# Performance work log

Hardware: AMD Instinct MI355X
Metric: run time of the kernel (lower is better)

## Reference

```python
import jax, jax.numpy as jnp
import numpy as np

P = 7    # pool size (hard-coded in module)
DS = 16  # downsample rate


def _hat_int(t):
    # antiderivative of the bilinear hat kernel max(0, 1-|t|)
    t = jnp.clip(t, -1.0, 1.0)
    return jnp.where(t < 0, 0.5 * (t + 1.0) ** 2, 1.0 - 0.5 * (1.0 - t) ** 2)


def _axis_weights(lo, hi, size):
    # Exact per-pixel integration weights for PrRoIPool along one axis.
    # lo, hi: [R] scaled roi coords. Returns W [R,P,size], bin width [R].
    bw = (hi - lo) / P
    starts = lo[:, None] + bw[:, None] * jnp.arange(P, dtype=lo.dtype)  # [R,P]
    ends = starts + bw[:, None]
    idx = jnp.arange(size, dtype=lo.dtype)
    W = _hat_int(ends[:, :, None] - idx) - _hat_int(starts[:, :, None] - idx)
    return W, bw


def prroi_pool(feat, rois):
    # Precise RoI pooling: exact integral of the bilinearly-interpolated feature
    # over each bin (separable -> two small matmuls). feat [C,H,W], rois [R,4].
    C, H, Wd = feat.shape
    s = 1.0 / DS
    Wx, bw = _axis_weights(rois[:, 0] * s, rois[:, 2] * s, Wd)
    Wy, bh = _axis_weights(rois[:, 1] * s, rois[:, 3] * s, H)
    pooled = jnp.einsum('chw,rph,rqw->rcpq', feat, Wy, Wx)  # [R,C,P,P]
    area = jnp.maximum(bw * bh, 1e-8)
    return pooled / area[:, None, None, None]


def intersection_map(box1, box2):
    # Fractional coverage of each PxP bin of box2's grid by box1 -> [N,1,P,P]
    bw = (box2[:, 2] - box2[:, 0]) / P
    bh = (box2[:, 3] - box2[:, 1]) / P
    gx0 = box2[:, 0, None] + bw[:, None] * jnp.arange(P)
    gy0 = box2[:, 1, None] + bh[:, None] * jnp.arange(P)
    ox = jnp.clip(jnp.minimum(gx0 + bw[:, None], box1[:, 2, None]) - jnp.maximum(gx0, box1[:, 0, None]), 0.0)
    oy = jnp.clip(jnp.minimum(gy0 + bh[:, None], box1[:, 3, None]) - jnp.maximum(gy0, box1[:, 1, None]), 0.0)
    frac = oy[:, :, None] * ox[:, None, :] / jnp.maximum(bw * bh, 1e-8)[:, None, None]
    return frac[:, None]


def conv1x1(x, W, b):
    # 1x1 conv as a channel matmul; x [...,C,H,W], W [D,C], b [D]
    return jnp.einsum('...chw,dc->...dhw', x, W) + b[:, None, None]


def setup_inputs() -> dict:
    key = jax.random.key(0)
    ks = jax.random.split(key, 12)
    B, C, Hf, Wf, n = 8, 256, 32, 32, 16
    D1 = D2 = 256
    inp = jax.random.normal(ks[0], (B, C, Hf, Wf), dtype=jnp.float32)
    N = B * n
    xy1 = jax.random.uniform(ks[1], (N, 2), dtype=jnp.float32) * 380.0
    wh = 40.0 + jax.random.uniform(ks[2], (N, 2), dtype=jnp.float32) * 90.0
    objects = jnp.concatenate([xy1, xy1 + wh], axis=-1)  # valid boxes inside 512x512
    objects_length = jnp.full((B,), n, dtype=jnp.int32)

    def kaiming(k, shape, fan_in):
        return jax.random.normal(k, shape, dtype=jnp.float32) * np.float32(np.sqrt(2.0 / fan_in))

    rin = C // 2 * 3 + 2 * D1
    return {
        'input': inp, 'objects': objects, 'objects_length': objects_length,
        'Wc': kaiming(ks[3], (C, C), C), 'bc': jnp.zeros((C,), jnp.float32),
        'Wr': kaiming(ks[4], (C // 2 * 3, C), C), 'br': jnp.zeros((C // 2 * 3,), jnp.float32),
        'Wof': kaiming(ks[5], (D1, 2 * C), 2 * C), 'bof': jnp.zeros((D1,), jnp.float32),
        'Wrf': kaiming(ks[6], (D2, rin), rin), 'brf': jnp.zeros((D2,), jnp.float32),
        'Wofc': kaiming(ks[7], (D1, D1 * P * P), D1 * P * P), 'bofc': jnp.zeros((D1,), jnp.float32),
        'Wrfc': kaiming(ks[8], (D2, D2 * P * P), D2 * P * P), 'brfc': jnp.zeros((D2,), jnp.float32),
    }


def reference(input, objects, objects_length, Wc, bc, Wr, br, Wof, bof, Wrf, brf, Wofc, bofc, Wrfc, brfc):
    B, C, H, Wd = input.shape
    n = objects.shape[0] // B  # uniform object count per image
    boxes = objects.reshape(B, n, 4)
    ctx_all = conv1x1(input, Wc, bc)           # [B,C,H,W]
    rel_all = conv1x1(input, Wr, br)           # [B,3C/2,H,W]
    img_box = jnp.array([0.0, 0.0, Wd * DS, H * DS], dtype=input.dtype)
    sub_id = jnp.repeat(jnp.arange(n), n)
    obj_id = jnp.tile(jnp.arange(n), n)

    def per_image(feat, ctx, rel, box):
        # context pooled over the full-image box is identical for all objects
        ctx_pool = prroi_pool(ctx, img_box[None])[0]                    # [C,P,P]
        x_c, y_c = jnp.split(ctx_pool, 2, axis=0)
        box_imap = jax.lax.stop_gradient(
            intersection_map(box, jnp.broadcast_to(img_box, (n, 4))))  # [n,1,P,P]
        obj_pool = prroi_pool(feat, box)                                # [n,C,P,P]
        obj_in = jnp.concatenate([
            obj_pool,
            jnp.broadcast_to(x_c, (n,) + x_c.shape),
            y_c[None] * box_imap], axis=1)                              # [n,2C,P,P]
        obj_feat = conv1x1(obj_in, Wof, bof)                            # [n,D1,P,P]

        sub_box, ob_box = box[sub_id], box[obj_id]                      # [n*n,4]
        union = jax.lax.stop_gradient(jnp.concatenate(
            [jnp.minimum(sub_box[:, :2], ob_box[:, :2]),
             jnp.maximum(sub_box[:, 2:], ob_box[:, 2:])], axis=-1))
        sub_imap = jax.lax.stop_gradient(intersection_map(sub_box, union))
        obj_imap = jax.lax.stop_gradient(intersection_map(ob_box, union))
        rel_pool = prroi_pool(rel, union)                               # [n*n,3C/2,P,P]
        xr, yr, zr = jnp.split(rel_pool, 3, axis=1)
        rel_in = jnp.concatenate([
            obj_feat[sub_id], obj_feat[obj_id],
            xr, yr * sub_imap, zr * obj_imap], axis=1)                  # [n*n,2D1+3C/2,P,P]
        rel_feat = conv1x1(rel_in, Wrf, brf)                            # [n*n,D2,P,P]

        o = jax.nn.relu(obj_feat).reshape(n, -1) @ Wofc.T + bofc
        o = o / jnp.linalg.norm(o, axis=-1, keepdims=True)
        r = jax.nn.relu(rel_feat).reshape(n * n, -1) @ Wrfc.T + brfc
        r = r / jnp.linalg.norm(r, axis=-1, keepdims=True)
        return o, r.reshape(n, n, -1)

    obj_out, rel_out = jax.vmap(per_image)(input, ctx_all, rel_all, boxes)
    return obj_out, rel_out
```

## Files before the change

kernel.cpp:

```cpp
#include <hip/hip_runtime.h>
#include <hip/hip_bf16.h>


#define Bimg 8
#define Cch 256
#define HW 1024
#define CREL 384
#define CCAT 640
#define KFC 12544
#define STS 236

typedef __hip_bfloat16 bf16;
typedef __attribute__((ext_vector_type(8))) short short8;
typedef __attribute__((ext_vector_type(4))) short short4_t;
typedef __attribute__((ext_vector_type(4))) float f32x4;

__device__ __forceinline__ float hat_int(float t) {
    t = fminf(1.f, fmaxf(-1.f, t));
    return (t < 0.f) ? 0.5f * (t + 1.f) * (t + 1.f) : 1.f - 0.5f * (1.f - t) * (1.f - t);
}
__device__ __forceinline__ float b2f(short s) {
    return __uint_as_float(((unsigned)(unsigned short)s) << 16);
}
__device__ __forceinline__ unsigned pack2bf(float a, float b) {
    bf16 ha = __float2bfloat16(a), hb = __float2bfloat16(b);
    return ((unsigned)(unsigned short)(*(short*)&hb) << 16) | (unsigned short)(*(short*)&ha);
}

__global__ void prep_k(const float* __restrict__ Wc, const float* __restrict__ bc,
                       const float* __restrict__ Wr, const float* __restrict__ br,
                       bf16* __restrict__ Wcat, float* __restrict__ bcat,
                       const float* __restrict__ Wof, bf16* __restrict__ wof16,
                       const float* __restrict__ Wrf, bf16* __restrict__ wasao16,
                       bf16* __restrict__ wrfxyz16) {
    int bid = blockIdx.x, tid = threadIdx.x;
    if (bid < 640) {
        int t = bid * 256 + tid;
        int d = t >> 8, c = t & 255;
        Wcat[t] = __float2bfloat16((d < 256) ? Wc[d * 256 + c] : Wr[(d - 256) * 256 + c]);
        if (t < CCAT) bcat[t] = (t < 256) ? bc[t] : br[t - 256];
    } else if (bid < 1152) {
        int t = (bid - 640) * 256 + tid;
        wof16[t] = __float2bfloat16(Wof[t]);
    } else if (bid < 1664) {
        int t = (bid - 1152) * 256 + tid;
        int m = t >> 8, k = t & 255;
        wasao16[t] = __float2bfloat16((m < 256) ? Wrf[m * 896 + k] : Wrf[(m - 256) * 896 + 256 + k]);
    } else {
        int t = (bid - 1664) * 256 + tid;
        int d = t / 384, k = t - d * 384;
        wrfxyz16[t] = __float2bfloat16(Wrf[d * 896 + 512 + k]);
    }
}
__global__ __launch_bounds__(256) void wfc_pack_k(const float* __restrict__ W, bf16* __restrict__ dst) {
    __shared__ float ld[64 * 50];
    int dout = blockIdx.y, d0 = blockIdx.x * 64;
    int tid = threadIdx.x;
    for (int e = tid; e < 64 * 49; e += 256) {
        int di = e / 49, pq = e - di * 49;
        ld[di * 50 + pq] = W[(size_t)dout * KFC + (d0 + di) * 49 + pq];
    }
    __syncthreads();
    for (int e = tid; e < 64 * 49; e += 256) {
        int pq = e >> 6, di = e & 63;
        if (pq < 49)
            dst[(size_t)dout * KFC + pq * 256 + d0 + di] = __float2bfloat16(ld[di * 50 + pq]);
    }
}

__global__ void axisw_k(const float* __restrict__ objects,
                        float* __restrict__ orec, float* __restrict__ urec,
                        float* __restrict__ crec, float* __restrict__ bimap) {
    int bid = blockIdx.x;
    float b0, b1, b2, b3;
    float* rec;
    const float *sbp = nullptr, *obp = nullptr;
    if (bid < 128) {
        b0 = objects[bid * 4]; b1 = objects[bid * 4 + 1];
        b2 = objects[bid * 4 + 2]; b3 = objects[bid * 4 + 3];
        rec = orec + (size_t)bid * 128;
    } else if (bid < 2176) {
        int u = bid - 128;
        int img = u >> 8, pair = u & 255, i = pair >> 4, j = pair & 15;
        sbp = objects + (img * 16 + i) * 4;
        obp = objects + (img * 16 + j) * 4;
        b0 = fminf(sbp[0], obp[0]); b1 = fminf(sbp[1], obp[1]);
        b2 = fmaxf(sbp[2], obp[2]); b3 = fmaxf(sbp[3], obp[3]);
        rec = urec + (size_t)(u) * 224;
    } else {
        b0 = 0.f; b1 = 0.f; b2 = 512.f; b3 = 512.f;
        rec = crec;
    }
    const float sc = 0.0625f;
    float lox = b0 * sc, bwx = (b2 * sc - lox) * (1.f / 7.f);
    float loy = b1 * sc, bwy = (b3 * sc - loy) * (1.f / 7.f);
    float ia = 1.f / fmaxf(bwx * bwy, 1e-8f);
    int tid = threadIdx.x;
    if (tid < 56) {
        int p = tid >> 3, k = tid & 7;
        {
            float st = loy + bwy * p, en = st + bwy;
            int h0 = min(max((int)floorf(st) - 1, 0), 24);
            rec[tid] = hat_int(en - (float)(h0 + k)) - hat_int(st - (float)(h0 + k));
            if (k == 0) ((int*)rec)[119 + p] = h0;
        }
        {
            float st = lox + bwx * p, en = st + bwx;
            int w0 = min(max((int)floorf(st) - 1, 0), 24);
            rec[56 + tid] = ia * (hat_int(en - (float)(w0 + k)) - hat_int(st - (float)(w0 + k)));
            if (k == 0) ((int*)rec)[112 + p] = w0;
        }
    }
    if (tid < 49) {
        int p = tid / 7, q = tid - p * 7;
        if (bid < 128) {
            float bw = 512.f / 7.f, bh = 512.f / 7.f;
            float gx0 = bw * q, gy0 = bh * p;
            float ox = fmaxf(fminf(gx0 + bw, b2) - fmaxf(gx0, b0), 0.f);
            float oy = fmaxf(fminf(gy0 + bh, b3) - fmaxf(gy0, b1), 0.f);
            bimap[bid * 49 + tid] = oy * ox / fmaxf(bw * bh, 1e-8f);
        } else if (bid < 2176) {
            float bw = (b2 - b0) * (1.f / 7.f), bh = (b3 - b1) * (1.f / 7.f);
            float gx0 = b0 + bw * q, gy0 = b1 + bh * p;
            float inv = 1.f / fmaxf(bw * bh, 1e-8f);
            float oxs = fmaxf(fminf(gx0 + bw, sbp[2]) - fmaxf(gx0, sbp[0]), 0.f);
            float oys = fmaxf(fminf(gy0 + bh, sbp[3]) - fmaxf(gy0, sbp[1]), 0.f);
            rec[126 + tid] = oys * oxs * inv;
            float oxo = fmaxf(fminf(gx0 + bw, obp[2]) - fmaxf(gx0, obp[0]), 0.f);
            float oyo = fmaxf(fminf(gy0 + bh, obp[3]) - fmaxf(gy0, obp[1]), 0.f);
            rec[175 + tid] = oyo * oxo * inv;
        }
    }
}

__global__ __launch_bounds__(256) void int_t_k(const float* __restrict__ input, bf16* __restrict__ intp) {
    __shared__ float st[64][65];
    int hw0 = blockIdx.x * 64, c0 = blockIdx.y * 64, b = blockIdx.z;
    int tid = threadIdx.x;
#pragma unroll
    for (int i = 0; i < 16; i++) {
        int e = tid + i * 256;
        int c = e >> 6, hw = e & 63;
        st[c][hw] = input[(size_t)b * 262144 + (size_t)(c0 + c) * 1024 + hw0 + hw];
    }
    __syncthreads();
#pragma unroll
    for (int i = 0; i < 16; i++) {
        int e = tid + i * 256;
        int hw = e >> 6, c = e & 63;
        intp[((size_t)b * 1024 + hw0 + hw) * 256 + c0 + c] = __float2bfloat16(st[c][hw]);
    }
}

__global__ __launch_bounds__(256) void mfma_gemm_k(
    const bf16* __restrict__ A, int lda,
    const bf16* __restrict__ BT, int ldbt,
    int Ktiles, int splitk, int mode,
    float* __restrict__ Cf, int Mtot, int Ntot,
    const float* __restrict__ bias,
    bf16* __restrict__ Ct, int ldct, bf16* __restrict__ Ct2) {
    __shared__ float tr[32 * 132];
    const int tid = threadIdx.x;
    const int m0 = blockIdx.y * 128, n0 = blockIdx.x * 128;
    int kz = blockIdx.z;
    const int tp = (Ktiles + splitk - 1) / splitk;
    const int kt0 = kz * tp;
    const int kt1 = min(Ktiles, kt0 + tp);
    const int lane = tid & 63, wid = tid >> 6;
    const int wm = (wid >> 1) * 64, wn = (wid & 1) * 64;
    const int lrow = lane & 15, lk = (lane >> 4) * 8;
    f32x4 acc[4][4];
#pragma unroll
    for (int i = 0; i < 4; i++)
#pragma unroll
        for (int j = 0; j < 4; j++) acc[i][j] = (f32x4){0.f, 0.f, 0.f, 0.f};
    const bf16* pA = A + (size_t)(m0 + wm + lrow) * lda + lk;
    const bf16* pB = BT + (size_t)(n0 + wn + lrow) * ldbt + lk;
    short8 a_c[4], b_c[4];
    if (kt0 < kt1) {
#pragma unroll
        for (int f = 0; f < 4; f++) {
            a_c[f] = *(const short8*)(pA + (size_t)f * 16 * lda + (size_t)kt0 * 32);
            b_c[f] = *(const short8*)(pB + (size_t)f * 16 * ldbt + (size_t)kt0 * 32);
        }
    }
    for (int kt = kt0; kt < kt1; kt++) {
        short8 a_n[4], b_n[4];
        if (kt + 1 < kt1) {
#pragma unroll
            for (int f = 0; f < 4; f++) {
                a_n[f] = *(const short8*)(pA + (size_t)f * 16 * lda + (size_t)(kt + 1) * 32);
                b_n[f] = *(const short8*)(pB + (size_t)f * 16 * ldbt + (size_t)(kt + 1) * 32);
            }
        }
#pragma unroll
        for (int i = 0; i < 4; i++)
#pragma unroll
            for (int j = 0; j < 4; j++)
                acc[i][j] = __builtin_amdgcn_mfma_f32_16x16x32_bf16(a_c[i], b_c[j], acc[i][j], 0, 0, 0);
#pragma unroll
        for (int f = 0; f < 4; f++) { a_c[f] = a_n[f]; b_c[f] = b_n[f]; }
    }
    const int rbase = (lane >> 4) * 4, cf = lane & 15;
    if (mode == 5) {
#pragma unroll
        for (int i = 0; i < 4; i++)
#pragma unroll
            for (int reg = 0; reg < 4; reg++) {
                int m = m0 + wm + i * 16 + rbase + reg;
                float bv = bias[m];
#pragma unroll
                for (int j = 0; j < 4; j++) {
                    int n = n0 + wn + j * 16 + cf;
                    Ct[(size_t)m * ldct + n] = __float2bfloat16(acc[i][j][reg] + bv);
                }
            }
        return;
    }
#pragma unroll 1
    for (int ci = 0; ci < 4; ci++) {
        __syncthreads();
        if ((wid & 1) == (ci >> 1)) {
            int jj0 = (ci & 1) * 2;
#pragma unroll
            for (int jj = jj0; jj < jj0 + 2; jj++)
#pragma unroll
                for (int i = 0; i < 4; i++)
#pragma unroll
                    for (int reg = 0; reg < 4; reg++) {
                        int nl = (wn + jj * 16 + cf) - 32 * ci;
                        int ml = wm + i * 16 + rbase + reg;
                        tr[nl * 132 + ml] = acc[i][jj][reg];
                    }
        }
        __syncthreads();
        if (mode == 2) {
            float* P = Cf + (size_t)kz * Mtot * Ntot;
            for (int e = tid; e < 1024; e += 256) {
                int nl = e >> 5, mq = (e & 31) * 4;
                int n = n0 + 32 * ci + nl;
                *(f32x4*)&P[(size_t)n * Mtot + m0 + mq] = *(f32x4*)&tr[nl * 132 + mq];
            }
        } else {
            for (int e = tid; e < 2048; e += 256) {
                int nl = e >> 6, mq = (e & 63) * 2;
                int n = n0 + 32 * ci + nl;
                int m = m0 + mq;
                float v0 = tr[nl * 132 + mq] + (bias ? bias[m] : 0.f);
                float v1 = tr[nl * 132 + mq + 1] + (bias ? bias[m + 1] : 0.f);
                *(unsigned*)&Ct[(size_t)n * ldct + m] = pack2bf(v0, v1);
                if (mode == 6) {
                    int r = n / 49, pq = n - r * 49;
                    *(unsigned*)&Ct2[(size_t)r * KFC + pq * 256 + m] =
                        pack2bf(fmaxf(v0, 0.f), fmaxf(v1, 0.f));
                }
            }
        }
    }
}

__global__ __launch_bounds__(256) void mfma_gemm256_k(
    const bf16* __restrict__ A, int lda,
    const bf16* __restrict__ BT, int ldbt, long zB,
    int Ktiles, int splitk, int mode,
    float* __restrict__ Cf, int Ntot,
    const float* __restrict__ bias,
    const bf16* __restrict__ ASAOT, int bimg0,
    bf16* __restrict__ Ct, long zC) {
    __shared__ float tr[16 * 260];
    const int tid = threadIdx.x;
    const int n0 = blockIdx.x * 64;
    int z = blockIdx.z;
    int kz = 0, bimg = bimg0;
    if (mode == 1) { BT += (size_t)z * zB; Ct += (size_t)z * zC; bimg = bimg0 + z; }
    else kz = z;
    const int tp = (Ktiles + splitk - 1) / splitk;
    const int kt0 = kz * tp;
    const int kt1 = min(Ktiles, kt0 + tp);
    const int lane = tid & 63, wid = tid >> 6;
    const int wm = wid * 64;
    const int lrow = lane & 15, lk = (lane >> 4) * 8;
    f32x4 acc[4][4];
#pragma unroll
    for (int i = 0; i < 4; i++)
#pragma unroll
        for (int j = 0; j < 4; j++) acc[i][j] = (f32x4){0.f, 0.f, 0.f, 0.f};
    const bf16* pA = A + (size_t)(wm + lrow) * lda + lk;
    const bf16* pB = (mode == 1)
        ? BT + (size_t)(lk >> 3) * 100352 + (size_t)(n0 + lrow) * 8
        : BT + (size_t)(n0 + lrow) * ldbt + lk;
    short8 a_c[4], b_c[4];
    if (kt0 < kt1) {
#pragma unroll
        for (int f = 0; f < 4; f++) {
            a_c[f] = *(const short8*)(pA + (size_t)f * 16 * lda + (size_t)kt0 * 32);
            b_c[f] = (mode == 1)
                ? *(const short8*)(pB + (size_t)kt0 * 4 * 100352 + f * 128)
                : *(const short8*)(pB + (size_t)f * 16 * ldbt + (size_t)kt0 * 32);
        }
    }
    for (int kt = kt0; kt < kt1; kt++) {
        short8 a_n[4], b_n[4];
        if (kt + 1 < kt1) {
#pragma unroll
            for (int f = 0; f < 4; f++) {
                a_n[f] = *(const short8*)(pA + (size_t)f * 16 * lda + (size_t)(kt + 1) * 32);
                b_n[f] = (mode == 1)
                    ? *(const short8*)(pB + (size_t)(kt + 1) * 4 * 100352 + f * 128)
                    : *(const short8*)(pB + (size_t)f * 16 * ldbt + (size_t)(kt + 1) * 32);
            }
        }
#pragma unroll
        for (int i = 0; i < 4; i++)
#pragma unroll
            for (int j = 0; j < 4; j++)
                acc[i][j] = __builtin_amdgcn_mfma_f32_16x16x32_bf16(a_c[i], b_c[j], acc[i][j], 0, 0, 0);
#pragma unroll
        for (int f = 0; f < 4; f++) { a_c[f] = a_n[f]; b_c[f] = b_n[f]; }
    }
    const int rbase = (lane >> 4) * 4, cf = lane & 15;
#pragma unroll 1
    for (int ci = 0; ci < 4; ci++) {
        __syncthreads();
#pragma unroll
        for (int i = 0; i < 4; i++)
#pragma unroll
            for (int reg = 0; reg < 4; reg++)
                tr[cf * 260 + wm + i * 16 + rbase + reg] = acc[i][ci][reg];
        __syncthreads();
        if (mode == 2) {
            float* P = Cf + (size_t)kz * 256 * Ntot;
            for (int e = tid; e < 1024; e += 256) {
                int nl = e >> 6, mq = (e & 63) * 4;
                int n = n0 + 16 * ci + nl;
                *(f32x4*)&P[(size_t)n * 256 + mq] = *(f32x4*)&tr[nl * 260 + mq];
            }
        } else {
            for (int e = tid; e < 512; e += 256) {
                int nl = e >> 5, mq = (e & 31) * 8;
                int n = n0 + 16 * ci + nl;
                int r = n / 49, pq = n - r * 49;
                int ii = r >> 4, jj2 = r & 15;
                const bf16* as = &ASAOT[((size_t)bimg * 784 + ii * 49 + pq) * 512 + mq];
                const bf16* ao = &ASAOT[((size_t)bimg * 784 + jj2 * 49 + pq) * 512 + 256 + mq];
                short8 pk;
#pragma unroll
                for (int u = 0; u < 8; u++) {
                    float v = tr[nl * 260 + mq + u] + bias[mq + u]
                            + b2f(*(const short*)&as[u]) + b2f(*(const short*)&ao[u]);
                    bf16 h = __float2bfloat16(fmaxf(v, 0.f));
                    pk[u] = *(short*)&h;
                }
                *(short8*)&Ct[(size_t)r * KFC + pq * 256 + mq] = pk;
            }
        }
    }
}

__global__ __launch_bounds__(256) void objpool_k(
    const float* __restrict__ input, const float* __restrict__ orec,
    bf16* __restrict__ objint) {
    int cg = blockIdx.x;
    int b = blockIdx.y;
    __shared__ float sF[8192];
    __shared__ float sT[2][1888];
    __shared__ float wb[2][128];
    int tid = threadIdx.x;
    const float* feat = input + (size_t)b * (Cch * HW) + (size_t)cg * 8 * HW;
    for (int e4 = tid; e4 < 2048; e4 += 256)
        *(f32x4*)&sF[e4 * 4] = *(const f32x4*)&feat[e4 * 4];
    const float* rb = orec + (size_t)b * 16 * 128;
    if (tid < 126) wb[0][tid] = rb[tid];
    int t1v = tid + 256;
    int c0 = tid / 56, r0 = tid - c0 * 56, p0 = r0 >> 3, w40 = r0 & 7;
    int c1 = t1v / 56, r1 = t1v - c1 * 56, p1 = r1 >> 3, w41 = r1 & 7;
    bool has1 = (t1v < 448);
    int sf0 = c0 * 1024 + w40 * 4, st0 = c0 * STS + p0 * 32 + w40 * 4;
    int sf1 = c1 * 1024 + w41 * 4, st1 = c1 * STS + p1 * 32 + w41 * 4;
    int xpq0 = tid >> 3, xc = tid & 7;
    int xp0 = xpq0 / 7, xq0 = xpq0 - xp0 * 7;
    int xpq1 = xpq0 + 32;
    int xp1 = xpq1 / 7, xq1 = xpq1 - xp1 * 7;
    bool xv1 = (xpq1 < 49);
    __syncthreads();
    for (int r2 = 0; r2 < 16; r2++) {
        const float* wc_ = wb[r2 & 1];
        float* stbuf = sT[r2 & 1];
        float pre;
        bool pf = (r2 < 15) && (tid < 126);
        if (pf) pre = rb[(r2 + 1) * 128 + tid];
        {
            int h0 = ((const int*)wc_)[119 + p0];
            const f32x4* f = (const f32x4*)&sF[sf0 + h0 * 32];
            f32x4 wya = *(const f32x4*)&wc_[p0 * 8];
            f32x4 wyb = *(const f32x4*)&wc_[p0 * 8 + 4];
            f32x4 a = f[0] * wya[0] + f[8] * wya[1] + f[16] * wya[2] + f[24] * wya[3]
                    + f[32] * wyb[0] + f[40] * wyb[1] + f[48] * wyb[2] + f[56] * wyb[3];
            *(f32x4*)&stbuf[st0] = a;
        }
        if (has1) {
            int h0 = ((const int*)wc_)[119 + p1];
            const f32x4* f = (const f32x4*)&sF[sf1 + h0 * 32];
            f32x4 wya = *(const f32x4*)&wc_[p1 * 8];
            f32x4 wyb = *(const f32x4*)&wc_[p1 * 8 + 4];
            f32x4 a = f[0] * wya[0] + f[8] * wya[1] + f[16] * wya[2] + f[24] * wya[3]
                    + f[32] * wyb[0] + f[40] * wyb[1] + f[48] * wyb[2] + f[56] * wyb[3];
            *(f32x4*)&stbuf[st1] = a;
        }
        f32x4 xwa0 = *(const f32x4*)&wc_[56 + xq0 * 8];
        f32x4 xwb0 = *(const f32x4*)&wc_[56 + xq0 * 8 + 4];
        int w0i0 = ((const int*)wc_)[112 + xq0];
        f32x4 xwa1 = {0, 0, 0, 0}, xwb1 = {0, 0, 0, 0};
        int w0i1 = 0;
        if (xv1) {
            xwa1 = *(const f32x4*)&wc_[56 + xq1 * 8];
            xwb1 = *(const f32x4*)&wc_[56 + xq1 * 8 + 4];
            w0i1 = ((const int*)wc_)[112 + xq1];
        }
        if (pf) wb[1 - (r2 & 1)][tid] = pre;
        __syncthreads();
        {
            bf16* orow = objint + ((size_t)b * 784 + (size_t)r2 * 49) * 512 + cg * 8 + xc;
            {
                const float* t = &stbuf[xc * STS + xp0 * 32 + w0i0];
                float s = t[0] * xwa0[0] + t[1] * xwa0[1] + t[2] * xwa0[2] + t[3] * xwa0[3]
                        + t[4] * xwb0[0] + t[5] * xwb0[1] + t[6] * xwb0[2] + t[7] * xwb0[3];
                orow[(size_t)xpq0 * 512] = __float2bfloat16(s);
            }
            if (xv1) {
                const float* t = &stbuf[xc * STS + xp1 * 32 + w0i1];
                float s = t[0] * xwa1[0] + t[1] * xwa1[1] + t[2] * xwa1[2] + t[3] * xwa1[3]
                        + t[4] * xwb1[0] + t[5] * xwb1[1] + t[6] * xwb1[2] + t[7] * xwb1[3];
                orow[(size_t)xpq1 * 512] = __float2bfloat16(s);
            }
        }
    }
}

__global__ __launch_bounds__(256) void ctxobjin_k(
    const bf16* __restrict__ ctxrelb, const float* __restrict__ crec,
    const float* __restrict__ bimap, bf16* __restrict__ objint) {
    int cg = blockIdx.x;
    int b = blockIdx.y;
    __shared__ float sF[8192];
    __shared__ float sT[1888];
    __shared__ float wc_[128];
    __shared__ float sBI[784];
    int tid = threadIdx.x;
    for (int e4 = tid; e4 < 2048; e4 += 256) {
        short4_t v = *(const short4_t*)&ctxrelb[(size_t)(cg * 8 + (e4 >> 8)) * 8192 + b * 1024 + (e4 & 255) * 4];
        f32x4 fv = {b2f(v[0]), b2f(v[1]), b2f(v[2]), b2f(v[3])};
        *(f32x4*)&sF[e4 * 4] = fv;
    }
    if (tid < 126) wc_[tid] = crec[tid];
    for (int e = tid; e < 784; e += 256) sBI[e] = bimap[b * 784 + e];
    __syncthreads();
    for (int tt = tid; tt < 448; tt += 256) {
        int c = tt / 56, r = tt - c * 56, p = r >> 3, w4 = r & 7;
        int h0 = ((const int*)wc_)[119 + p];
        const f32x4* f = (const f32x4*)&sF[c * 1024 + w4 * 4 + h0 * 32];
        f32x4 wya = *(const f32x4*)&wc_[p * 8];
        f32x4 wyb = *(const f32x4*)&wc_[p * 8 + 4];
        f32x4 a = f[0] * wya[0] + f[8] * wya[1] + f[16] * wya[2] + f[24] * wya[3]
                + f[32] * wyb[0] + f[40] * wyb[1] + f[48] * wyb[2] + f[56] * wyb[3];
        *(f32x4*)&sT[c * STS + p * 32 + w4 * 4] = a;
    }
    __syncthreads();
    bool scale = (cg >= 16);
    for (int e = tid; e < 392; e += 256) {
        int pq = e >> 3, c = e & 7;
        int p = pq / 7, q = pq - p * 7;
        int w0i = ((const int*)wc_)[112 + q];
        const float* t = &sT[c * STS + p * 32 + w0i];
        const f32x4* wx4 = (const f32x4*)&wc_[56 + q * 8];
        f32x4 a = wx4[0], b2 = wx4[1];
        float s = t[0] * a[0] + t[1] * a[1] + t[2] * a[2] + t[3] * a[3]
                + t[4] * b2[0] + t[5] * b2[1] + t[6] * b2[2] + t[7] * b2[3];
        int j = cg * 8 + c;
        bf16* orow = objint + ((size_t)b * 784 + pq) * 512 + 256 + j;
#pragma unroll
        for (int r = 0; r < 16; r++) {
            float m = scale ? sBI[r * 49 + pq] : 1.f;
            orow[(size_t)r * 49 * 512] = __float2bfloat16(s * m);
        }
    }
}

__global__ __launch_bounds__(256) void relpool_k(
    const bf16* __restrict__ ctxrelb, const float* __restrict__ urec,
    bf16* __restrict__ mbt, int b0) {
    int cg = blockIdx.x;
    int rg = blockIdx.y;
    int zi = blockIdx.z;
    int b = b0 + zi;
    mbt += (size_t)zi * 4816896;
    __shared__ float sF[8192];
    __shared__ float sT[2][1888];
    __shared__ float wb[2][224];
    int tid = threadIdx.x;
    for (int e4 = tid; e4 < 2048; e4 += 256) {
        short4_t v = *(const short4_t*)&ctxrelb[(size_t)(256 + cg * 8 + (e4 >> 8)) * 8192 + b * 1024 + (e4 & 255) * 4];
        f32x4 fv = {b2f(v[0]), b2f(v[1]), b2f(v[2]), b2f(v[3])};
        *(f32x4*)&sF[e4 * 4] = fv;
    }
    const float* rb = urec + ((size_t)b * 256 + (size_t)rg * 16) * 224;
    if (tid < 224) wb[0][tid] = rb[tid];
    int t1v = tid + 256;
    int c0 = tid / 56, r0 = tid - c0 * 56, p0 = r0 >> 3, w40 = r0 & 7;
    int c1 = t1v / 56, r1 = t1v - c1 * 56, p1 = r1 >> 3, w41 = r1 & 7;
    bool has1 = (t1v < 448);
    int sf0 = c0 * 1024 + w40 * 4, st0 = c0 * STS + p0 * 32 + w40 * 4;
    int sf1 = c1 * 1024 + w41 * 4, st1 = c1 * STS + p1 * 32 + w41 * 4;
    int xpq0 = tid >> 3, xc = tid & 7;
    int xp0 = xpq0 / 7, xq0 = xpq0 - xp0 * 7;
    int xpq1 = xpq0 + 32;
    int xp1 = xpq1 / 7, xq1 = xpq1 - xp1 * 7;
    bool xv1 = (xpq1 < 49);
    int cglob = cg * 8 + xc;
    int mclass = (cglob >= 256) ? 2 : (cglob >= 128 ? 1 : 0);
    __syncthreads();
    for (int r2 = 0; r2 < 16; r2++) {
        const float* wc_ = wb[r2 & 1];
        float* stbuf = sT[r2 & 1];
        float pre;
        bool pf = (r2 < 15) && (tid < 224);
        if (pf) pre = rb[(r2 + 1) * 224 + tid];
        {
            int h0 = ((const int*)wc_)[119 + p0];
            const f32x4* f = (const f32x4*)&sF[sf0 + h0 * 32];
            f32x4 wya = *(const f32x4*)&wc_[p0 * 8];
            f32x4 wyb = *(const f32x4*)&wc_[p0 * 8 + 4];
            f32x4 a = f[0] * wya[0] + f[8] * wya[1] + f[16] * wya[2] + f[24] * wya[3]
                    + f[32] * wyb[0] + f[40] * wyb[1] + f[48] * wyb[2] + f[56] * wyb[3];
            *(f32x4*)&stbuf[st0] = a;
        }
        if (has1) {
            int h0 = ((const int*)wc_)[119 + p1];
            const f32x4* f = (const f32x4*)&sF[sf1 + h0 * 32];
            f32x4 wya = *(const f32x4*)&wc_[p1 * 8];
            f32x4 wyb = *(const f32x4*)&wc_[p1 * 8 + 4];
            f32x4 a = f[0] * wya[0] + f[8] * wya[1] + f[16] * wya[2] + f[24] * wya[3]
                    + f[32] * wyb[0] + f[40] * wyb[1] + f[48] * wyb[2] + f[56] * wyb[3];
            *(f32x4*)&stbuf[st1] = a;
        }
        f32x4 xwa0 = *(const f32x4*)&wc_[56 + xq0 * 8];
        f32x4 xwb0 = *(const f32x4*)&wc_[56 + xq0 * 8 + 4];
        int w0i0 = ((const int*)wc_)[112 + xq0];
        float mul0 = (mclass == 2) ? wc_[175 + xpq0] : (mclass == 1 ? wc_[126 + xpq0] : 1.f);
        f32x4 xwa1 = {0, 0, 0, 0}, xwb1 = {0, 0, 0, 0};
        int w0i1 = 0;
        float mul1 = 1.f;
        if (xv1) {
            xwa1 = *(const f32x4*)&wc_[56 + xq1 * 8];
            xwb1 = *(const f32x4*)&wc_[56 + xq1 * 8 + 4];
            w0i1 = ((const int*)wc_)[112 + xq1];
            mul1 = (mclass == 2) ? wc_[175 + xpq1] : (mclass == 1 ? wc_[126 + xpq1] : 1.f);
        }
        if (pf) wb[1 - (r2 & 1)][tid] = pre;
        __syncthreads();
        {
            int r = rg * 16 + r2;
            bf16* orow = mbt + (size_t)cg * 100352 + (size_t)r * 392;
            {
                const float* t = &stbuf[xc * STS + xp0 * 32 + w0i0];
                float s = t[0] * xwa0[0] + t[1] * xwa0[1] + t[2] * xwa0[2] + t[3] * xwa0[3]
                        + t[4] * xwb0[0] + t[5] * xwb0[1] + t[6] * xwb0[2] + t[7] * xwb0[3];
                orow[xpq0 * 8 + xc] = __float2bfloat16(s * mul0);
            }
            if (xv1) {
                const float* t = &stbuf[xc * STS + xp1 * 32 + w0i1];
                float s = t[0] * xwa1[0] + t[1] * xwa1[1] + t[2] * xwa1[2] + t[3] * xwa1[3]
                        + t[4] * xwb1[0] + t[5] * xwb1[1] + t[6] * xwb1[2] + t[7] * xwb1[3];
                orow[xpq1 * 8 + xc] = __float2bfloat16(s * mul1);
            }
        }
    }
}

__global__ void redns_k(const float* __restrict__ Pd, const float* __restrict__ bias,
                        float* __restrict__ out, int N, int splitk, long outBase) {
    int vec = blockIdx.x, m = threadIdx.x;
    float s = bias[m];
    for (int z = 0; z < splitk; z++) s += Pd[(size_t)z * 256 * N + (size_t)vec * 256 + m];
    float ss = s * s;
    for (int o = 32; o > 0; o >>= 1) ss += __shfl_down(ss, o, 64);
    __shared__ float red[4];
    if ((m & 63) == 0) red[m >> 6] = ss;
    __syncthreads();
    float tot = red[0] + red[1] + red[2] + red[3];
    out[outBase + (size_t)vec * 256 + m] = s / sqrtf(tot);
}

extern "C" void kernel_launch(void* const* d_in, const int* in_sizes, int n_in,
                              void* d_out, int out_size, void* d_ws, size_t ws_size,
                              hipStream_t stream) {
    const float* input = (const float*)d_in[0];
    const float* objects = (const float*)d_in[1];
    const float* Wc = (const float*)d_in[3];
    const float* bc = (const float*)d_in[4];
    const float* Wr = (const float*)d_in[5];
    const float* br = (const float*)d_in[6];
    const float* Wof = (const float*)d_in[7];
    const float* bof = (const float*)d_in[8];
    const float* Wrf = (const float*)d_in[9];
    const float* brf = (const float*)d_in[10];
    const float* Wofc = (const float*)d_in[11];
    const float* bofc = (const float*)d_in[12];
    const float* Wrfc = (const float*)d_in[13];
    const float* brfc = (const float*)d_in[14];
    float* out = (float*)d_out;

    float* w = (float*)d_ws;
    bf16* WCAT16   = (bf16*)(w + 0);
    float* BCAT    = w + 81920;
    bf16* CTXRELB  = (bf16*)(w + 82560);
    float* OREC    = w + 2704000;
    float* UREC    = w + 2720384;
    float* CREC    = w + 3179136;
    float* BIMAP   = w + 3179264;
    bf16* ASAOT16  = (bf16*)(w + 3185536);
    bf16* WRFXYZ16 = (bf16*)(w + 4791168);
    bf16* WRFC16   = (bf16*)(w + 4840320);
    float* OVL     = w + 6445952;
    bf16* INT16    = (bf16*)(OVL + 0);
    bf16* WOF16    = (bf16*)(OVL + 1048576);
    bf16* WASAO16  = (bf16*)(OVL + 1114112);
    bf16* WOFC16   = (bf16*)(OVL + 1179648);
    bf16* OBJINT   = (bf16*)(OVL + 2785280);
    bf16* OBJFT    = (bf16*)(OVL + 4390912);
    bf16* XOT      = (bf16*)(OVL + 5193728);
    float* OPART   = OVL + 5996544;
    bf16* MBT4     = (bf16*)(OVL + 0);
    float* RPART   = OVL + 0;
    bf16* XBT4     = (bf16*)(OVL + 9633792);

    prep_k<<<dim3(2048), 256, 0, stream>>>(Wc, bc, Wr, br, WCAT16, BCAT,
                                           Wof, WOF16, Wrf, WASAO16, WRFXYZ16);
    wfc_pack_k<<<dim3(4, 256), 256, 0, stream>>>(Wrfc, WRFC16);
    wfc_pack_k<<<dim3(4, 256), 256, 0, stream>>>(Wofc, WOFC16);
    axisw_k<<<dim3(2177), 64, 0, stream>>>(objects, OREC, UREC, CREC, BIMAP);
    int_t_k<<<dim3(16, 4, 8), 256, 0, stream>>>(input, INT16);
    mfma_gemm_k<<<dim3(64, 5, 1), 256, 0, stream>>>(WCAT16, 256, INT16, 256, 8, 1, 5,
                                                    nullptr, 640, 8192, BCAT,
                                                    CTXRELB, 8192, nullptr);
    objpool_k<<<dim3(32, 8), 256, 0, stream>>>(input, OREC, OBJINT);
    ctxobjin_k<<<dim3(32, 8), 256, 0, stream>>>(CTXRELB, CREC, BIMAP, OBJINT);
    mfma_gemm_k<<<dim3(49, 2, 1), 256, 0, stream>>>(WOF16, 512, OBJINT, 512, 16, 1, 6,
                                                    nullptr, 256, 6272, bof,
                                                    OBJFT, 256, XOT);
    mfma_gemm_k<<<dim3(49, 4, 1), 256, 0, stream>>>(WASAO16, 256, OBJFT, 256, 8, 1, 3,
                                                    nullptr, 512, 6272, nullptr,
                                                    ASAOT16, 512, nullptr);
    mfma_gemm_k<<<dim3(1, 2, 56), 256, 0, stream>>>(WOFC16, KFC, XOT, KFC, 392, 56, 2,
                                                    OPART, 256, 128, nullptr,
                                                    nullptr, 0, nullptr);
    redns_k<<<dim3(128), 256, 0, stream>>>(OPART, bofc, out, 128, 56, 0L);

    for (int g = 0; g < 2; g++) {
        int b0 = g * 4;
        relpool_k<<<dim3(48, 16, 4), 256, 0, stream>>>(CTXRELB, UREC, MBT4, b0);
        mfma_gemm256_k<<<dim3(196, 1, 4), 256, 0, stream>>>(WRFXYZ16, 384, MBT4, 384, 4816896L,
                                                            12, 1, 1,
                                                            nullptr, KFC, brf,
                                                            ASAOT16, b0, XBT4, 3211264L);
        mfma_gemm256_k<<<dim3(16, 1, 24), 256, 0, stream>>>(WRFC16, KFC, XBT4, KFC, 0L,
                                                            392, 24, 2,
                                                            RPART, 1024, nullptr,
                                                            nullptr, 0, nullptr, 0L);
        redns_k<<<dim3(1024), 256, 0, stream>>>(RPART, brfc, out, 1024, 24,
                                                32768L + (long)g * 262144L);
    }
}
```

Before: 652.1 us.

## Exploit union-box symmetry to pool each subject/object pair once in relpool

Result: faster. 618.4 us (median of 2 runs) (-5.2%).

```diff
diff --git a/kernel.cpp b/kernel.cpp
--- a/kernel.cpp
+++ b/kernel.cpp
@@ -25,6 +25,11 @@
 __device__ __forceinline__ unsigned pack2bf(float a, float b) {
     bf16 ha = __float2bfloat16(a), hb = __float2bfloat16(b);
     return ((unsigned)(unsigned short)(*(short*)&hb) << 16) | (unsigned short)(*(short*)&ha);
+}
+__device__ __forceinline__ void u2pair(int u, int& oi, int& oj) {
+    int ii = 0, base = 0;
+    while (u >= base + 16 - ii) { base += 16 - ii; ii++; }
+    oi = ii; oj = ii + (u - base);
 }
 
 __global__ void prep_k(const float* __restrict__ Wc, const float* __restrict__ bc,
@@ -503,8 +508,11 @@
         f32x4 fv = {b2f(v[0]), b2f(v[1]), b2f(v[2]), b2f(v[3])};
         *(f32x4*)&sF[e4 * 4] = fv;
     }
-    const float* rb = urec + ((size_t)b * 256 + (size_t)rg * 16) * 224;
-    if (tid < 224) wb[0][tid] = rb[tid];
+    const float* rb = urec + (size_t)b * 256 * 224;
+    {
+        int i0, j0; u2pair(rg * 8, i0, j0);
+        if (tid < 224) wb[0][tid] = rb[(size_t)(i0 * 16 + j0) * 224 + tid];
+    }
     int t1v = tid + 256;
     int c0 = tid / 56, r0 = tid - c0 * 56, p0 = r0 >> 3, w40 = r0 & 7;
     int c1 = t1v / 56, r1 = t1v - c1 * 56, p1 = r1 >> 3, w41 = r1 & 7;
@@ -519,12 +527,16 @@
     int cglob = cg * 8 + xc;
     int mclass = (cglob >= 256) ? 2 : (cglob >= 128 ? 1 : 0);
     __syncthreads();
-    for (int r2 = 0; r2 < 16; r2++) {
+    for (int r2 = 0; r2 < 8; r2++) {
         const float* wc_ = wb[r2 & 1];
         float* stbuf = sT[r2 & 1];
+        int pi, pj; u2pair(rg * 8 + r2, pi, pj);
         float pre;
-        bool pf = (r2 < 15) && (tid < 224);
-        if (pf) pre = rb[(r2 + 1) * 224 + tid];
+        bool pf = (r2 < 7) && (tid < 224);
+        if (pf) {
+            int ni, nj; u2pair(rg * 8 + r2 + 1, ni, nj);
+            pre = rb[(size_t)(ni * 16 + nj) * 224 + tid];
+        }
         {
             int h0 = ((const int*)wc_)[119 + p0];
             const f32x4* f = (const f32x4*)&sF[sf0 + h0 * 32];
@@ -546,32 +558,40 @@
         f32x4 xwa0 = *(const f32x4*)&wc_[56 + xq0 * 8];
         f32x4 xwb0 = *(const f32x4*)&wc_[56 + xq0 * 8 + 4];
         int w0i0 = ((const int*)wc_)[112 + xq0];
-        float mul0 = (mclass == 2) ? wc_[175 + xpq0] : (mclass == 1 ? wc_[126 + xpq0] : 1.f);
+        float si0 = wc_[126 + xpq0], oi0 = wc_[175 + xpq0];
+        float mA0 = (mclass == 1) ? si0 : (mclass == 2 ? oi0 : 1.f);
+        float mB0 = (mclass == 1) ? oi0 : (mclass == 2 ? si0 : 1.f);
         f32x4 xwa1 = {0, 0, 0, 0}, xwb1 = {0, 0, 0, 0};
         int w0i1 = 0;
-        float mul1 = 1.f;
+        float mA1 = 1.f, mB1 = 1.f;
         if (xv1) {
             xwa1 = *(const f32x4*)&wc_[56 + xq1 * 8];
             xwb1 = *(const f32x4*)&wc_[56 + xq1 * 8 + 4];
             w0i1 = ((const int*)wc_)[112 + xq1];
-            mul1 = (mclass == 2) ? wc_[175 + xpq1] : (mclass == 1 ? wc_[126 + xpq1] : 1.f);
+            float si1 = wc_[126 + xpq1], oi1 = wc_[175 + xpq1];
+            mA1 = (mclass == 1) ? si1 : (mclass == 2 ? oi1 : 1.f);
+            mB1 = (mclass == 1) ? oi1 : (mclass == 2 ? si1 : 1.f);
         }
         if (pf) wb[1 - (r2 & 1)][tid] = pre;
         __syncthreads();
         {
-            int r = rg * 16 + r2;
-            bf16* orow = mbt + (size_t)cg * 100352 + (size_t)r * 392;
+            int rA = pi * 16 + pj, rB = pj * 16 + pi;
+            bf16* baseA = mbt + (size_t)cg * 100352 + (size_t)rA * 392;
+            bf16* baseB = mbt + (size_t)cg * 100352 + (size_t)rB * 392;
+            bool dual = (pi != pj);
             {
                 const float* t = &stbuf[xc * STS + xp0 * 32 + w0i0];
                 float s = t[0] * xwa0[0] + t[1] * xwa0[1] + t[2] * xwa0[2] + t[3] * xwa0[3]
                         + t[4] * xwb0[0] + t[5] * xwb0[1] + t[6] * xwb0[2] + t[7] * xwb0[3];
-                orow[xpq0 * 8 + xc] = __float2bfloat16(s * mul0);
+                baseA[xpq0 * 8 + xc] = __float2bfloat16(s * mA0);
+                if (dual) baseB[xpq0 * 8 + xc] = __float2bfloat16(s * mB0);
             }
             if (xv1) {
                 const float* t = &stbuf[xc * STS + xp1 * 32 + w0i1];
                 float s = t[0] * xwa1[0] + t[1] * xwa1[1] + t[2] * xwa1[2] + t[3] * xwa1[3]
                         + t[4] * xwb1[0] + t[5] * xwb1[1] + t[6] * xwb1[2] + t[7] * xwb1[3];
-                orow[xpq1 * 8 + xc] = __float2bfloat16(s * mul1);
+                baseA[xpq1 * 8 + xc] = __float2bfloat16(s * mA1);
+                if (dual) baseB[xpq1 * 8 + xc] = __float2bfloat16(s * mB1);
             }
         }
     }
@@ -658,7 +678,7 @@
 
     for (int g = 0; g < 2; g++) {
         int b0 = g * 4;
-        relpool_k<<<dim3(48, 16, 4), 256, 0, stream>>>(CTXRELB, UREC, MBT4, b0);
+        relpool_k<<<dim3(48, 17, 4), 256, 0, stream>>>(CTXRELB, UREC, MBT4, b0);
         mfma_gemm256_k<<<dim3(196, 1, 4), 256, 0, stream>>>(WRFXYZ16, 384, MBT4, 384, 4816896L,
                                                             12, 1, 1,
                                                             nullptr, KFC, brf,
```
